# Performance work log

Hardware: AMD Instinct MI355X
Metric: run time of the kernel (lower is better)

## Reference

```python
import jax, jax.numpy as jnp
import numpy as np

B, L, H = 256, 2048, 64

def _min_gru(x, Wz, bz, Wh, bh):
    # x: [B, L, Din] -> h: [B, L, H] via parallel scan of h_t = (1-z_t)*h_{t-1} + z_t*h~_t, h_0 = 0
    z = jax.nn.sigmoid(jnp.einsum('bli,ih->blh', x, Wz) + bz)
    h_tilde = jnp.einsum('bli,ih->blh', x, Wh) + bh
    a = 1.0 - z
    b = z * h_tilde
    def combine(c1, c2):
        a1, b1 = c1
        a2, b2 = c2
        return a1 * a2, b1 * a2 + b2
    _, h = jax.lax.associative_scan(combine, (a, b), axis=1)
    return h

def _stacked(x, Wz0, bz0, Wh0, bh0, Wz1, bz1, Wh1, bh1, Wo, bo):
    h = _min_gru(x, Wz0, bz0, Wh0, bh0)
    h = _min_gru(h, Wz1, bz1, Wh1, bh1)
    return jnp.einsum('blh,ho->blo', h, Wo) + bo  # [B, L, 1]

def setup_inputs():
    key = jax.random.key(0)
    ks = jax.random.split(key, 32)
    inputs = jax.random.bernoulli(ks[0], 0.5, (B, L)).astype(jnp.float32)
    p_array = jax.random.permutation(ks[1], L).astype(jnp.int32)
    def lin(k, fin, fout):
        return (jax.random.normal(k, (fin, fout), jnp.float32) / np.float32(np.sqrt(fin)))
    d = {'inputs': inputs, 'p_array': p_array}
    i = 2
    for r in (1, 2):
        for nm, fin, fout in (('z0', 1, H), ('h0', 1, H), ('z1', H, H), ('h1', H, H), ('o', H, 1)):
            d['w%d%s' % (r, nm)] = lin(ks[i], fin, fout); i += 1
            d['b%d%s' % (r, nm)] = jnp.zeros((fout,), jnp.float32)
    return d

def reference(inputs, p_array, w1z0, b1z0, w1h0, b1h0, w1z1, b1z1, w1h1, b1h1, w1o, b1o,
              w2z0, b2z0, w2h0, b2h0, w2z1, b2z1, w2h1, b2h1, w2o, b2o):
    x = inputs[..., None]                      # [B, L, 1]
    x_sys = _stacked(x, w1z0, b1z0, w1h0, b1h0, w1z1, b1z1, w1h1, b1h1, w1o, b1o)
    x_int = x[:, p_array, :]                   # interleave along sequence dim
    x_p1 = _stacked(x_int, w2z0, b2z0, w2h0, b2h0, w2z1, b2z1, w2h1, b2h1, w2o, b2o)
    x_tx = jnp.concatenate([x_sys, x_p1], axis=2)  # [B, L, 2]
    mean = jnp.mean(x_tx)
    std = jnp.std(x_tx, ddof=1)                # torch.std is unbiased by default
    return (x_tx - mean) / std                 # squeeze(dim=2) is a no-op on size-2 dim
```

## Files before the change

kernel.cpp:

```cpp
#include <hip/hip_runtime.h>

#define BB 256
#define LL 2048
#define HH 64
#define TT 64
#define SS 68
#define NCH (LL / TT)
#define NTOT (BB * LL * 2)

typedef __attribute__((ext_vector_type(8))) short bf16x8;
typedef __attribute__((ext_vector_type(4))) float f32x4;

__device__ __forceinline__ float sigmoidf_(float v) {
    return 1.0f / (1.0f + __expf(-v));
}
__device__ __forceinline__ short f2bf(float f) {
    union { float f; unsigned u; } v; v.f = f;
    unsigned r = v.u + 0x7fff + ((v.u >> 16) & 1);
    return (short)(r >> 16);
}
__device__ __forceinline__ float bf2f(short s) {
    union { unsigned u; float f; } v;
    v.u = ((unsigned)(unsigned short)s) << 16;
    return v.f;
}

template<int CTRL>
__device__ __forceinline__ float qdpp(float x) {
    union { float f; int i; } u, r;
    u.f = x;
    r.i = __builtin_amdgcn_update_dpp(0, u.i, CTRL, 0xF, 0xF, false);
    return r.f;
}

__device__ __forceinline__ void load_x(const float* __restrict__ xrow,
                                       const int* __restrict__ p,
                                       bool pm, int tb, float* xv)
{
    if (!pm) {
        const float4* x4 = (const float4*)(xrow + tb);
        #pragma unroll
        for (int k = 0; k < 4; ++k) {
            const float4 v = x4[k];
            xv[4*k+0] = v.x; xv[4*k+1] = v.y; xv[4*k+2] = v.z; xv[4*k+3] = v.w;
        }
    } else {
        const int4* p4 = (const int4*)(p + tb);
        int idx[16];
        #pragma unroll
        for (int k = 0; k < 4; ++k) {
            const int4 v = p4[k];
            idx[4*k+0] = v.x; idx[4*k+1] = v.y; idx[4*k+2] = v.z; idx[4*k+3] = v.w;
        }
        #pragma unroll
        for (int i = 0; i < 16; ++i) xv[i] = xrow[idx[i]];
    }
}

__device__ __forceinline__ void p1_scan(const float* xv,
                                        float a0v, float b0v, float a1v, float b1v,
                                        int seg, int col0, float& carry, float* sh)
{
    float ai[16], bi[16];
    float A = 1.0f, Bv = 0.0f;
    #pragma unroll
    for (int i = 0; i < 16; ++i) {
        const bool on = (xv[i] != 0.0f);
        ai[i] = on ? a1v : a0v;
        bi[i] = on ? b1v : b0v;
        A  = A * ai[i];
        Bv = fmaf(Bv, ai[i], bi[i]);
    }
    {
        const float Au = qdpp<0x90>(A), Bu = qdpp<0x90>(Bv);
        if (seg >= 1) { const float Ac = A; A = Au * Ac; Bv = fmaf(Bu, Ac, Bv); }
        const float Au2 = qdpp<0x44>(A), Bu2 = qdpp<0x44>(Bv);
        if (seg >= 2) { const float Ac = A; A = Au2 * Ac; Bv = fmaf(Bu2, Ac, Bv); }
    }
    float Ae = qdpp<0x90>(A), Be = qdpp<0x90>(Bv);
    if (seg == 0) { Ae = 1.0f; Be = 0.0f; }
    float cc = fmaf(Ae, carry, Be);
    #pragma unroll
    for (int i = 0; i < 16; ++i) {
        cc = fmaf(ai[i], cc, bi[i]);
        sh[(seg * 16 + i) * SS + col0] = cc;
    }
    carry = qdpp<0xFF>(cc);
}

__device__ __forceinline__ float reduce16_quadgroups(const float* v, int m) {
    float a[8];
    #pragma unroll
    for (int k = 0; k < 8; ++k) {
        const float keep = (m & 1) ? v[2*k+1] : v[2*k];
        const float send = (m & 1) ? v[2*k]   : v[2*k+1];
        a[k] = keep + __shfl_xor(send, 4);
    }
    float b2[4];
    #pragma unroll
    for (int k = 0; k < 4; ++k) {
        const float keep = (m & 2) ? a[2*k+1] : a[2*k];
        const float send = (m & 2) ? a[2*k]   : a[2*k+1];
        b2[k] = keep + __shfl_xor(send, 8);
    }
    float c2[2];
    #pragma unroll
    for (int k = 0; k < 2; ++k) {
        const float keep = (m & 4) ? b2[2*k+1] : b2[2*k];
        const float send = (m & 4) ? b2[2*k]   : b2[2*k+1];
        c2[k] = keep + __shfl_xor(send, 16);
    }
    const float keep = (m & 8) ? c2[1] : c2[0];
    const float send = (m & 8) ? c2[0] : c2[1];
    return keep + __shfl_xor(send, 32);
}

__global__ void __launch_bounds__(256)
__attribute__((amdgpu_waves_per_eu(2, 2)))
gru_fused(const float* __restrict__ x, const int* __restrict__ p,
               const float* __restrict__ w1z0, const float* __restrict__ b1z0,
               const float* __restrict__ w1h0, const float* __restrict__ b1h0,
               const float* __restrict__ w1z1, const float* __restrict__ b1z1,
               const float* __restrict__ w1h1, const float* __restrict__ b1h1,
               const float* __restrict__ w1o,  const float* __restrict__ b1o,
               const float* __restrict__ w2z0, const float* __restrict__ b2z0,
               const float* __restrict__ w2h0, const float* __restrict__ b2h0,
               const float* __restrict__ w2z1, const float* __restrict__ b2z1,
               const float* __restrict__ w2h1, const float* __restrict__ b2h1,
               const float* __restrict__ w2o,  const float* __restrict__ b2o,
               float* __restrict__ out, float* __restrict__ ws)
{
    const int  b  = blockIdx.x;
    const bool pm = (blockIdx.y != 0);

    const float* wz0 = pm ? w2z0 : w1z0;
    const float* bz0 = pm ? b2z0 : b1z0;
    const float* wh0 = pm ? w2h0 : w1h0;
    const float* bh0 = pm ? b2h0 : b1h0;
    const float* wz1 = pm ? w2z1 : w1z1;
    const float* bz1 = pm ? b2z1 : b1z1;
    const float* wh1 = pm ? w2h1 : w1h1;
    const float* bh1 = pm ? b2h1 : b1h1;
    const float* wo  = pm ? w2o  : w1o;
    const float* bov = pm ? b2o  : b1o;

    const int tid  = threadIdx.x;
    const int lane = tid & 63;
    const int tg   = tid >> 6;
    const int q    = lane >> 4;
    const int n    = lane & 15;
    const int seg  = lane & 3;
    const int hidx = (tg << 4) | (lane >> 2);

    __shared__ __align__(16) float s_h[TT * SS];
    __shared__ __align__(16) float s_at[HH * SS];
    __shared__ __align__(16) float s_bt[HH * SS];
    __shared__ float s_p[4 * TT];

    const float* xrow = x + (size_t)b * LL;

    const float z0v = sigmoidf_(bz0[hidx]);
    const float z1v = sigmoidf_(wz0[hidx] + bz0[hidx]);
    const float a0v = 1.0f - z0v, b0v = z0v * bh0[hidx];
    const float a1v = 1.0f - z1v, b1v = z1v * (wh0[hidx] + bh0[hidx]);

    float rbz1[4], rbh1[4];
    #pragma unroll
    for (int ht = 0; ht < 4; ++ht) {
        rbz1[ht] = bz1[ht * 16 + n];
        rbh1[ht] = bh1[ht * 16 + n];
    }
    const float bo   = bov[0];
    const float rwoh = wo[hidx];

    bf16x8 wfz_hi[2][4], wfh_hi[2][4];
    for (int ks = 0; ks < 2; ++ks) {
        for (int ht = 0; ht < 4; ++ht) {
            #pragma unroll
            for (int j = 0; j < 8; ++j) {
                const int kk = ks * 32 + q * 8 + j;
                const int hh = ht * 16 + n;
                wfz_hi[ks][ht][j] = f2bf(wz1[kk * HH + hh]);
                wfh_hi[ks][ht][j] = f2bf(wh1[kk * HH + hh]);
            }
        }
    }

    float carry0 = 0.0f, carry1 = 0.0f;
    float lsum = 0.0f, lsum2 = 0.0f;
    float* outp = out + (pm ? 1 : 0);
    const int t0 = tg * 16;
    const int col0 = hidx ^ ((seg & 1) << 4);

    float xv[16];

    load_x(xrow, p, pm, seg * 16, xv);
    p1_scan(xv, a0v, b0v, a1v, b1v, seg, col0, carry0, s_h);
    __syncthreads();

    for (int c = 0; c < NCH; ++c) {
        const int cp1 = c + 1;

        if (cp1 < NCH)
            load_x(xrow, p, pm, cp1 * TT + seg * 16, xv);

        if (c > 0 && tid < TT) {
            const float v = s_p[tid] + s_p[64 + tid] + s_p[128 + tid] + s_p[192 + tid] + bo;
            outp[((size_t)b * LL + (c - 1) * TT + tid) * 2] = v;
            lsum += v;
            lsum2 = fmaf(v, v, lsum2);
        }

        {
            f32x4 accz[4], acch[4];
            #pragma unroll
            for (int ht = 0; ht < 4; ++ht) {
                accz[ht] = (f32x4){rbz1[ht], rbz1[ht], rbz1[ht], rbz1[ht]};
                acch[ht] = (f32x4){rbh1[ht], rbh1[ht], rbh1[ht], rbh1[ht]};
            }
            const int qs = q ^ ((tg & 1) << 1);
            #pragma unroll
            for (int ks = 0; ks < 2; ++ks) {
                const float* ap = &s_h[(t0 + n) * SS + ks * 32 + qs * 8];
                const float4 av0 = *(const float4*)ap;
                const float4 av1 = *(const float4*)(ap + 4);
                float af[8] = {av0.x, av0.y, av0.z, av0.w, av1.x, av1.y, av1.z, av1.w};
                bf16x8 ahi, alo;
                #pragma unroll
                for (int j = 0; j < 8; ++j) {
                    const short h16 = f2bf(af[j]);
                    ahi[j] = h16;
                    alo[j] = f2bf(af[j] - bf2f(h16));
                }
                #pragma unroll
                for (int ht = 0; ht < 4; ++ht) {
                    accz[ht] = __builtin_amdgcn_mfma_f32_16x16x32_bf16(ahi, wfz_hi[ks][ht], accz[ht], 0, 0, 0);
                    accz[ht] = __builtin_amdgcn_mfma_f32_16x16x32_bf16(alo, wfz_hi[ks][ht], accz[ht], 0, 0, 0);
                    acch[ht] = __builtin_amdgcn_mfma_f32_16x16x32_bf16(ahi, wfh_hi[ks][ht], acch[ht], 0, 0, 0);
                    acch[ht] = __builtin_amdgcn_mfma_f32_16x16x32_bf16(alo, wfh_hi[ks][ht], acch[ht], 0, 0, 0);
                }
            }
            const int cbw = 4 * ((tg * 4 + q) ^ (n & 3));
            #pragma unroll
            for (int ht = 0; ht < 4; ++ht) {
                float4 av, bv4;
                float* avp = (float*)&av; float* bvp = (float*)&bv4;
                #pragma unroll
                for (int r = 0; r < 4; ++r) {
                    const float z = sigmoidf_(accz[ht][r]);
                    avp[r] = 1.0f - z;
                    bvp[r] = z * acch[ht][r];
                }
                const int row = ht * 16 + n;
                *(float4*)&s_at[row * SS + cbw] = av;
                *(float4*)&s_bt[row * SS + cbw] = bv4;
            }
        }
        __syncthreads();

        {
            float ai[16], bi[16];
            #pragma unroll
            for (int j4 = 0; j4 < 4; ++j4) {
                const int cb = 4 * ((seg * 4 + j4) ^ (hidx & 3));
                const float4 av = *(const float4*)&s_at[hidx * SS + cb];
                const float4 bv = *(const float4*)&s_bt[hidx * SS + cb];
                ai[4*j4+0] = av.x; ai[4*j4+1] = av.y; ai[4*j4+2] = av.z; ai[4*j4+3] = av.w;
                bi[4*j4+0] = bv.x; bi[4*j4+1] = bv.y; bi[4*j4+2] = bv.z; bi[4*j4+3] = bv.w;
            }
            float A = 1.0f, Bv = 0.0f;
            #pragma unroll
            for (int i = 0; i < 16; ++i) {
                A  = A * ai[i];
                Bv = fmaf(Bv, ai[i], bi[i]);
            }
            {
                const float Au = qdpp<0x90>(A), Bu = qdpp<0x90>(Bv);
                if (seg >= 1) { const float Ac = A; A = Au * Ac; Bv = fmaf(Bu, Ac, Bv); }
                const float Au2 = qdpp<0x44>(A), Bu2 = qdpp<0x44>(Bv);
                if (seg >= 2) { const float Ac = A; A = Au2 * Ac; Bv = fmaf(Bu2, Ac, Bv); }
            }
            float Ae = qdpp<0x90>(A), Be = qdpp<0x90>(Bv);
            if (seg == 0) { Ae = 1.0f; Be = 0.0f; }
            float cc = fmaf(Ae, carry1, Be);
            float pt[16];
            #pragma unroll
            for (int i = 0; i < 16; ++i) {
                cc = fmaf(ai[i], cc, bi[i]);
                pt[i] = cc * rwoh;
            }
            carry1 = qdpp<0xFF>(cc);
            const float r = reduce16_quadgroups(pt, lane >> 2);
            s_p[tg * 64 + seg * 16 + (lane >> 2)] = r;
        }

        if (cp1 < NCH)
            p1_scan(xv, a0v, b0v, a1v, b1v, seg, col0, carry0, s_h);
        __syncthreads();
    }

    if (tid < TT) {
        const float v = s_p[tid] + s_p[64 + tid] + s_p[128 + tid] + s_p[192 + tid] + bo;
        outp[((size_t)b * LL + (NCH - 1) * TT + tid) * 2] = v;
        lsum += v;
        lsum2 = fmaf(v, v, lsum2);
    }

    if (tg == 0) {
        #pragma unroll
        for (int o = 32; o; o >>= 1) {
            lsum  += __shfl_down(lsum, o);
            lsum2 += __shfl_down(lsum2, o);
        }
        if (lane == 0) {
            const int gb = b * 2 + (pm ? 1 : 0);
            ws[2 * gb]     = lsum;
            ws[2 * gb + 1] = lsum2;
        }
    }
}

__global__ void normalize_k(float* __restrict__ out, const float* __restrict__ ws)
{
    __shared__ float s_red[8];
    float s = 0.0f, s2 = 0.0f;
    for (int i = threadIdx.x; i < 2 * BB; i += 256) {
        s  += ws[2 * i];
        s2 += ws[2 * i + 1];
    }
    #pragma unroll
    for (int o = 32; o; o >>= 1) {
        s  += __shfl_down(s, o);
        s2 += __shfl_down(s2, o);
    }
    const int wid = threadIdx.x >> 6;
    if ((threadIdx.x & 63) == 0) { s_red[wid] = s; s_red[4 + wid] = s2; }
    __syncthreads();
    const float tot  = s_red[0] + s_red[1] + s_red[2] + s_red[3];
    const float tot2 = s_red[4] + s_red[5] + s_red[6] + s_red[7];
    const float N    = (float)NTOT;
    const float mean = tot / N;
    const float var  = (tot2 - N * mean * mean) / (N - 1.0f);
    const float inv  = rsqrtf(var);

    const int i = blockIdx.x * blockDim.x + threadIdx.x;
    float4* o4 = (float4*)out;
    float4 v = o4[i];
    v.x = (v.x - mean) * inv;
    v.y = (v.y - mean) * inv;
    v.z = (v.z - mean) * inv;
    v.w = (v.w - mean) * inv;
    o4[i] = v;
}

extern "C" void kernel_launch(void* const* d_in, const int* in_sizes, int n_in,
                              void* d_out, int out_size, void* d_ws, size_t ws_size,
                              hipStream_t stream)
{
    (void)in_sizes; (void)n_in; (void)out_size; (void)ws_size;
    const float* x = (const float*)d_in[0];
    const int*   p = (const int*)d_in[1];
    float* out = (float*)d_out;
    float* ws  = (float*)d_ws;

    dim3 grid(BB, 2);
    gru_fused<<<grid, 256, 0, stream>>>(
        x, p,
        (const float*)d_in[2],  (const float*)d_in[3],
        (const float*)d_in[4],  (const float*)d_in[5],
        (const float*)d_in[6],  (const float*)d_in[7],
        (const float*)d_in[8],  (const float*)d_in[9],
        (const float*)d_in[10], (const float*)d_in[11],
        (const float*)d_in[12], (const float*)d_in[13],
        (const float*)d_in[14], (const float*)d_in[15],
        (const float*)d_in[16], (const float*)d_in[17],
        (const float*)d_in[18], (const float*)d_in[19],
        (const float*)d_in[20], (const float*)d_in[21],
        out, ws);

    normalize_k<<<NTOT / 4 / 256, 256, 0, stream>>>(out, ws);
}
```

Measured before the change: 222.1 us.

## Scan layer-2 gates directly in MFMA registers, dropping LDS transpose and barrier

The second-layer scan now runs directly on the MFMA accumulator layout. Each lane scans its 4 rows, quad-groups combine through shuffles, and per-wave chunk summaries go through a small double-buffered LDS array. This removes the s_at/s_bt transpose through shared memory, one __syncthreads per chunk and the quad-group reduction. s_h is double-buffered so the layer-1 scan can write the next chunk while MFMA reads the current one. It also adds truncation-based bf16 splitting and an rcp-based sigmoid. These trade some rounding accuracy for fewer instructions, and the output reduction moves to shuffles with a deferred step.

```diff
diff --git a/kernel.cpp b/kernel.cpp
--- a/kernel.cpp
+++ b/kernel.cpp
@@ -11,18 +11,12 @@
 typedef __attribute__((ext_vector_type(8))) short bf16x8;
 typedef __attribute__((ext_vector_type(4))) float f32x4;
 
-__device__ __forceinline__ float sigmoidf_(float v) {
-    return 1.0f / (1.0f + __expf(-v));
-}
-__device__ __forceinline__ short f2bf(float f) {
+__device__ __forceinline__ float rcp_(float x) { return __builtin_amdgcn_rcpf(x); }
+
+__device__ __forceinline__ short f2bf_rne(float f) {
     union { float f; unsigned u; } v; v.f = f;
     unsigned r = v.u + 0x7fff + ((v.u >> 16) & 1);
     return (short)(r >> 16);
-}
-__device__ __forceinline__ float bf2f(short s) {
-    union { unsigned u; float f; } v;
-    v.u = ((unsigned)(unsigned short)s) << 16;
-    return v.f;
 }
 
 template<int CTRL>
@@ -86,33 +80,6 @@
         sh[(seg * 16 + i) * SS + col0] = cc;
     }
     carry = qdpp<0xFF>(cc);
-}
-
-__device__ __forceinline__ float reduce16_quadgroups(const float* v, int m) {
-    float a[8];
-    #pragma unroll
-    for (int k = 0; k < 8; ++k) {
-        const float keep = (m & 1) ? v[2*k+1] : v[2*k];
-        const float send = (m & 1) ? v[2*k]   : v[2*k+1];
-        a[k] = keep + __shfl_xor(send, 4);
-    }
-    float b2[4];
-    #pragma unroll
-    for (int k = 0; k < 4; ++k) {
-        const float keep = (m & 2) ? a[2*k+1] : a[2*k];
-        const float send = (m & 2) ? a[2*k]   : a[2*k+1];
-        b2[k] = keep + __shfl_xor(send, 8);
-    }
-    float c2[2];
-    #pragma unroll
-    for (int k = 0; k < 2; ++k) {
-        const float keep = (m & 4) ? b2[2*k+1] : b2[2*k];
-        const float send = (m & 4) ? b2[2*k]   : b2[2*k+1];
-        c2[k] = keep + __shfl_xor(send, 16);
-    }
-    const float keep = (m & 8) ? c2[1] : c2[0];
-    const float send = (m & 8) ? c2[0] : c2[1];
-    return keep + __shfl_xor(send, 32);
 }
 
 __global__ void __launch_bounds__(256)
@@ -152,41 +119,43 @@
     const int seg  = lane & 3;
     const int hidx = (tg << 4) | (lane >> 2);
 
-    __shared__ __align__(16) float s_h[TT * SS];
-    __shared__ __align__(16) float s_at[HH * SS];
-    __shared__ __align__(16) float s_bt[HH * SS];
-    __shared__ float s_p[4 * TT];
+    __shared__ __align__(16) float s_h[2 * TT * SS];
+    __shared__ float2 s_w[2][4][HH];
+    __shared__ float s_red[8];
 
     const float* xrow = x + (size_t)b * LL;
 
-    const float z0v = sigmoidf_(bz0[hidx]);
-    const float z1v = sigmoidf_(wz0[hidx] + bz0[hidx]);
+    const float z0v = rcp_(1.0f + __expf(-bz0[hidx]));
+    const float z1v = rcp_(1.0f + __expf(-(wz0[hidx] + bz0[hidx])));
     const float a0v = 1.0f - z0v, b0v = z0v * bh0[hidx];
     const float a1v = 1.0f - z1v, b1v = z1v * (wh0[hidx] + bh0[hidx]);
 
-    float rbz1[4], rbh1[4];
+    float rbz1[4], rbh1[4], rwo4[4];
     #pragma unroll
     for (int ht = 0; ht < 4; ++ht) {
         rbz1[ht] = bz1[ht * 16 + n];
         rbh1[ht] = bh1[ht * 16 + n];
-    }
-    const float bo   = bov[0];
-    const float rwoh = wo[hidx];
-
-    bf16x8 wfz_hi[2][4], wfh_hi[2][4];
+        rwo4[ht] = wo[ht * 16 + n];
+    }
+    const float bo = bov[0];
+
+    bf16x8 wfz[2][4], wfh[2][4];
     for (int ks = 0; ks < 2; ++ks) {
         for (int ht = 0; ht < 4; ++ht) {
             #pragma unroll
             for (int j = 0; j < 8; ++j) {
                 const int kk = ks * 32 + q * 8 + j;
                 const int hh = ht * 16 + n;
-                wfz_hi[ks][ht][j] = f2bf(wz1[kk * HH + hh]);
-                wfh_hi[ks][ht][j] = f2bf(wh1[kk * HH + hh]);
-            }
-        }
-    }
-
-    float carry0 = 0.0f, carry1 = 0.0f;
+                wfz[ks][ht][j] = f2bf_rne(wz1[kk * HH + hh]);
+                wfh[ks][ht][j] = f2bf_rne(wh1[kk * HH + hh]);
+            }
+        }
+    }
+
+    float carry0 = 0.0f;
+    float carry1[4] = {0.0f, 0.0f, 0.0f, 0.0f};
+    f32x4 ga[4], gb[4];
+    float Aqe[4], Bqe[4];
     float lsum = 0.0f, lsum2 = 0.0f;
     float* outp = out + (pm ? 1 : 0);
     const int t0 = tg * 16;
@@ -194,6 +163,47 @@
 
     float xv[16];
 
+    auto g2_step = [&](int cm) {
+        const int buf = cm & 1;
+        float Acm[4] = {1,1,1,1}, Bcm[4] = {0,0,0,0};
+        float Ap[4], Bp[4];
+        #pragma unroll
+        for (int w = 0; w < 4; ++w) {
+            #pragma unroll
+            for (int ht = 0; ht < 4; ++ht) {
+                if (w == tg) { Ap[ht] = Acm[ht]; Bp[ht] = Bcm[ht]; }
+                const float2 ab = s_w[buf][w][ht * 16 + n];
+                Bcm[ht] = fmaf(ab.x, Bcm[ht], ab.y);
+                Acm[ht] *= ab.x;
+            }
+        }
+        float vo[4] = {0,0,0,0};
+        #pragma unroll
+        for (int ht = 0; ht < 4; ++ht) {
+            float cc = fmaf(Aqe[ht], fmaf(Ap[ht], carry1[ht], Bp[ht]), Bqe[ht]);
+            #pragma unroll
+            for (int r = 0; r < 4; ++r) {
+                cc = fmaf(ga[ht][r], cc, gb[ht][r]);
+                vo[r] = fmaf(cc, rwo4[ht], vo[r]);
+            }
+            carry1[ht] = fmaf(Acm[ht], carry1[ht], Bcm[ht]);
+        }
+        #pragma unroll
+        for (int m = 1; m <= 8; m <<= 1) {
+            #pragma unroll
+            for (int r = 0; r < 4; ++r) vo[r] += __shfl_xor(vo[r], m);
+        }
+        if (n == 0) {
+            #pragma unroll
+            for (int r = 0; r < 4; ++r) {
+                const float v = vo[r] + bo;
+                outp[((size_t)b * LL + cm * TT + t0 + q * 4 + r) * 2] = v;
+                lsum += v;
+                lsum2 = fmaf(v, v, lsum2);
+            }
+        }
+    };
+
     load_x(xrow, p, pm, seg * 16, xv);
     p1_scan(xv, a0v, b0v, a1v, b1v, seg, col0, carry0, s_h);
     __syncthreads();
@@ -204,119 +214,105 @@
         if (cp1 < NCH)
             load_x(xrow, p, pm, cp1 * TT + seg * 16, xv);
 
-        if (c > 0 && tid < TT) {
-            const float v = s_p[tid] + s_p[64 + tid] + s_p[128 + tid] + s_p[192 + tid] + bo;
-            outp[((size_t)b * LL + (c - 1) * TT + tid) * 2] = v;
-            lsum += v;
-            lsum2 = fmaf(v, v, lsum2);
-        }
+        if (c > 0) g2_step(c - 1);
 
         {
-            f32x4 accz[4], acch[4];
-            #pragma unroll
-            for (int ht = 0; ht < 4; ++ht) {
-                accz[ht] = (f32x4){rbz1[ht], rbz1[ht], rbz1[ht], rbz1[ht]};
-                acch[ht] = (f32x4){rbh1[ht], rbh1[ht], rbh1[ht], rbh1[ht]};
-            }
+            #pragma unroll
+            for (int ht = 0; ht < 4; ++ht) {
+                ga[ht] = (f32x4){rbz1[ht], rbz1[ht], rbz1[ht], rbz1[ht]};
+                gb[ht] = (f32x4){rbh1[ht], rbh1[ht], rbh1[ht], rbh1[ht]};
+            }
+            const float* shR = s_h + (c & 1) * (TT * SS);
             const int qs = q ^ ((tg & 1) << 1);
             #pragma unroll
             for (int ks = 0; ks < 2; ++ks) {
-                const float* ap = &s_h[(t0 + n) * SS + ks * 32 + qs * 8];
+                const float* ap = &shR[(t0 + n) * SS + ks * 32 + qs * 8];
                 const float4 av0 = *(const float4*)ap;
                 const float4 av1 = *(const float4*)(ap + 4);
                 float af[8] = {av0.x, av0.y, av0.z, av0.w, av1.x, av1.y, av1.z, av1.w};
                 bf16x8 ahi, alo;
                 #pragma unroll
                 for (int j = 0; j < 8; ++j) {
-                    const short h16 = f2bf(af[j]);
-                    ahi[j] = h16;
-                    alo[j] = f2bf(af[j] - bf2f(h16));
+                    union { float f; unsigned u; } uf; uf.f = af[j];
+                    ahi[j] = (short)(uf.u >> 16);
+                    union { unsigned u; float f; } hf; hf.u = uf.u & 0xffff0000u;
+                    const float rem = af[j] - hf.f;
+                    union { float f; unsigned u; } ur; ur.f = rem;
+                    alo[j] = (short)(ur.u >> 16);
                 }
                 #pragma unroll
                 for (int ht = 0; ht < 4; ++ht) {
-                    accz[ht] = __builtin_amdgcn_mfma_f32_16x16x32_bf16(ahi, wfz_hi[ks][ht], accz[ht], 0, 0, 0);
-                    accz[ht] = __builtin_amdgcn_mfma_f32_16x16x32_bf16(alo, wfz_hi[ks][ht], accz[ht], 0, 0, 0);
-                    acch[ht] = __builtin_amdgcn_mfma_f32_16x16x32_bf16(ahi, wfh_hi[ks][ht], acch[ht], 0, 0, 0);
-                    acch[ht] = __builtin_amdgcn_mfma_f32_16x16x32_bf16(alo, wfh_hi[ks][ht], acch[ht], 0, 0, 0);
+                    ga[ht] = __builtin_amdgcn_mfma_f32_16x16x32_bf16(ahi, wfz[ks][ht], ga[ht], 0, 0, 0);
+                    ga[ht] = __builtin_amdgcn_mfma_f32_16x16x32_bf16(alo, wfz[ks][ht], ga[ht], 0, 0, 0);
+                    gb[ht] = __builtin_amdgcn_mfma_f32_16x16x32_bf16(ahi, wfh[ks][ht], gb[ht], 0, 0, 0);
+                    gb[ht] = __builtin_amdgcn_mfma_f32_16x16x32_bf16(alo, wfh[ks][ht], gb[ht], 0, 0, 0);
                 }
             }
-            const int cbw = 4 * ((tg * 4 + q) ^ (n & 3));
-            #pragma unroll
-            for (int ht = 0; ht < 4; ++ht) {
-                float4 av, bv4;
-                float* avp = (float*)&av; float* bvp = (float*)&bv4;
+            #pragma unroll
+            for (int ht = 0; ht < 4; ++ht) {
                 #pragma unroll
                 for (int r = 0; r < 4; ++r) {
-                    const float z = sigmoidf_(accz[ht][r]);
-                    avp[r] = 1.0f - z;
-                    bvp[r] = z * acch[ht][r];
+                    const float v  = ga[ht][r];
+                    const float e  = __expf(-v);
+                    const float r1 = rcp_(1.0f + e);
+                    ga[ht][r] = e * r1;
+                    gb[ht][r] = r1 * gb[ht][r];
                 }
-                const int row = ht * 16 + n;
-                *(float4*)&s_at[row * SS + cbw] = av;
-                *(float4*)&s_bt[row * SS + cbw] = bv4;
-            }
-        }
+            }
+            float Aq[4], Bq[4];
+            #pragma unroll
+            for (int ht = 0; ht < 4; ++ht) {
+                float A = 1.0f, B = 0.0f;
+                #pragma unroll
+                for (int r = 0; r < 4; ++r) {
+                    B = fmaf(ga[ht][r], B, gb[ht][r]);
+                    A = A * ga[ht][r];
+                }
+                Aq[ht] = A; Bq[ht] = B;
+            }
+            #pragma unroll
+            for (int ht = 0; ht < 4; ++ht) {
+                const float Au = __shfl_up(Aq[ht], 16), Bu = __shfl_up(Bq[ht], 16);
+                if (q >= 1) { const float Ac = Aq[ht]; Aq[ht] = Ac * Au; Bq[ht] = fmaf(Ac, Bu, Bq[ht]); }
+            }
+            #pragma unroll
+            for (int ht = 0; ht < 4; ++ht) {
+                const float Au = __shfl_up(Aq[ht], 32), Bu = __shfl_up(Bq[ht], 32);
+                if (q >= 2) { const float Ac = Aq[ht]; Aq[ht] = Ac * Au; Bq[ht] = fmaf(Ac, Bu, Bq[ht]); }
+            }
+            #pragma unroll
+            for (int ht = 0; ht < 4; ++ht) {
+                const float Ae = __shfl_up(Aq[ht], 16), Be = __shfl_up(Bq[ht], 16);
+                Aqe[ht] = (q == 0) ? 1.0f : Ae;
+                Bqe[ht] = (q == 0) ? 0.0f : Be;
+            }
+            if (q == 3) {
+                #pragma unroll
+                for (int ht = 0; ht < 4; ++ht)
+                    s_w[c & 1][tg][ht * 16 + n] = make_float2(Aq[ht], Bq[ht]);
+            }
+        }
+
+        if (cp1 < NCH)
+            p1_scan(xv, a0v, b0v, a1v, b1v, seg, col0, carry0,
+                    s_h + (cp1 & 1) * (TT * SS));
+
         __syncthreads();
-
-        {
-            float ai[16], bi[16];
-            #pragma unroll
-            for (int j4 = 0; j4 < 4; ++j4) {
-                const int cb = 4 * ((seg * 4 + j4) ^ (hidx & 3));
-                const float4 av = *(const float4*)&s_at[hidx * SS + cb];
-                const float4 bv = *(const float4*)&s_bt[hidx * SS + cb];
-                ai[4*j4+0] = av.x; ai[4*j4+1] = av.y; ai[4*j4+2] = av.z; ai[4*j4+3] = av.w;
-                bi[4*j4+0] = bv.x; bi[4*j4+1] = bv.y; bi[4*j4+2] = bv.z; bi[4*j4+3] = bv.w;
-            }
-            float A = 1.0f, Bv = 0.0f;
-            #pragma unroll
-            for (int i = 0; i < 16; ++i) {
-                A  = A * ai[i];
-                Bv = fmaf(Bv, ai[i], bi[i]);
-            }
-            {
-                const float Au = qdpp<0x90>(A), Bu = qdpp<0x90>(Bv);
-                if (seg >= 1) { const float Ac = A; A = Au * Ac; Bv = fmaf(Bu, Ac, Bv); }
-                const float Au2 = qdpp<0x44>(A), Bu2 = qdpp<0x44>(Bv);
-                if (seg >= 2) { const float Ac = A; A = Au2 * Ac; Bv = fmaf(Bu2, Ac, Bv); }
-            }
-            float Ae = qdpp<0x90>(A), Be = qdpp<0x90>(Bv);
-            if (seg == 0) { Ae = 1.0f; Be = 0.0f; }
-            float cc = fmaf(Ae, carry1, Be);
-            float pt[16];
-            #pragma unroll
-            for (int i = 0; i < 16; ++i) {
-                cc = fmaf(ai[i], cc, bi[i]);
-                pt[i] = cc * rwoh;
-            }
-            carry1 = qdpp<0xFF>(cc);
-            const float r = reduce16_quadgroups(pt, lane >> 2);
-            s_p[tg * 64 + seg * 16 + (lane >> 2)] = r;
-        }
-
-        if (cp1 < NCH)
-            p1_scan(xv, a0v, b0v, a1v, b1v, seg, col0, carry0, s_h);
-        __syncthreads();
-    }
-
-    if (tid < TT) {
-        const float v = s_p[tid] + s_p[64 + tid] + s_p[128 + tid] + s_p[192 + tid] + bo;
-        outp[((size_t)b * LL + (NCH - 1) * TT + tid) * 2] = v;
-        lsum += v;
-        lsum2 = fmaf(v, v, lsum2);
-    }
-
-    if (tg == 0) {
-        #pragma unroll
-        for (int o = 32; o; o >>= 1) {
-            lsum  += __shfl_down(lsum, o);
-            lsum2 += __shfl_down(lsum2, o);
-        }
-        if (lane == 0) {
-            const int gb = b * 2 + (pm ? 1 : 0);
-            ws[2 * gb]     = lsum;
-            ws[2 * gb + 1] = lsum2;
-        }
+    }
+
+    g2_step(NCH - 1);
+
+    #pragma unroll
+    for (int o = 32; o; o >>= 1) {
+        lsum  += __shfl_down(lsum, o);
+        lsum2 += __shfl_down(lsum2, o);
+    }
+    if (lane == 0) { s_red[tg] = lsum; s_red[4 + tg] = lsum2; }
+    __syncthreads();
+    if (tid == 0) {
+        const int gb2 = b * 2 + (pm ? 1 : 0);
+        ws[2 * gb2]     = s_red[0] + s_red[1] + s_red[2] + s_red[3];
+        ws[2 * gb2 + 1] = s_red[4] + s_red[5] + s_red[6] + s_red[7];
     }
 }
 
```

Measured after the change: 212.6 us. -4.3%, faster.
